# Performance work log

Hardware: AMD Instinct MI355X
Metric: run time of the kernel (lower is better)

The kernel has to match this reference:

```python
import jax, jax.numpy as jnp
import numpy as np

# ---- static geometry (matches init_kwargs) ----
B, S, D = 2, 4096, 2048
H, HD = 32, 64                      # num_heads, head_dim
HGRID, WGRID = 64, 64               # canvas h_dim, w_dim
TH, TW = 8, 16                      # tile size (th*tw = 128)
KH, KW = 16, 32                     # window (kernel) size
NTH, NTW = HGRID // TH, WGRID // TW
T = NTH * NTW                       # 32 tiles
TN = TH * TW                        # 128 tokens per tile
KTH, KTW = KH // TH, KW // TW
K = KTH * KTW                       # 4 kv tiles per query tile
SCALE = 1.0 / np.sqrt(HD)


def _kv_tile_ids():
    # For each query tile, the K kv tiles inside its (clamped) sliding window.
    qt = np.arange(T)
    qh, qw = qt // NTW, qt % NTW
    lbh, rbh = KTH // 2, KTH // 2 + (KTH % 2 - 1)
    lbw, rbw = KTW // 2, KTW // 2 + (KTW % 2 - 1)
    ch = np.clip(qh, lbh, NTH - 1 - rbh)
    cw = np.clip(qw, lbw, NTW - 1 - rbw)
    hh = ch[:, None] - lbh + np.arange(KTH)          # [T, KTH]
    ww = cw[:, None] - lbw + np.arange(KTW)          # [T, KTW]
    return (hh[:, :, None] * NTW + ww[:, None, :]).reshape(T, K)

KV_TILES = jnp.asarray(_kv_tile_ids())  # [T, K] int


def _to_tiles(x):
    # [B, S, H, HD] (row-major h,w) -> [B, H, T, TN, HD] (tile-major)
    x = x.reshape(B, NTH, TH, NTW, TW, H, HD)
    x = x.transpose(0, 5, 1, 3, 2, 4, 6)  # B,H,nth,ntw,th,tw,hd
    return x.reshape(B, H, T, TN, HD)


def _from_tiles(x):
    # [B, H, T, TN, HD] -> [B, S, H*HD]
    x = x.reshape(B, H, NTH, NTW, TH, TW, HD)
    x = x.transpose(0, 2, 4, 3, 5, 1, 6)  # B,nth,th,ntw,tw,H,hd
    return x.reshape(B, S, H * HD)


def setup_inputs() -> dict:
    key = jax.random.key(0)
    ks = jax.random.split(key, 5)
    sw = 1.0 / np.sqrt(D)
    return {
        "hidden_states": jax.random.normal(ks[0], (B, S, D), jnp.float32),
        "Wq": jax.random.normal(ks[1], (D, D), jnp.float32) * sw,
        "Wk": jax.random.normal(ks[2], (D, D), jnp.float32) * sw,
        "Wv": jax.random.normal(ks[3], (D, D), jnp.float32) * sw,
        "Wo": jax.random.normal(ks[4], (D, D), jnp.float32) * sw,
    }


def reference(hidden_states, Wq, Wk, Wv, Wo):
    # projections (weights stored [in, out]; equivalent to nn.Linear math)
    q = _to_tiles((hidden_states @ Wq).reshape(B, S, H, HD))  # [B,H,T,TN,HD]
    k = _to_tiles((hidden_states @ Wk).reshape(B, S, H, HD))
    v = _to_tiles((hidden_states @ Wv).reshape(B, S, H, HD))

    # gather the K allowed kv tiles for every query tile (block-sparse pattern)
    kg = k[:, :, KV_TILES].reshape(B, H, T, K * TN, HD)  # [B,H,T,K*TN,HD]
    vg = v[:, :, KV_TILES].reshape(B, H, T, K * TN, HD)

    # dense attention within each block (all gathered tokens are valid)
    scores = jnp.einsum("bhtqd,bhtkd->bhtqk", q, kg) * SCALE
    attn = jax.nn.softmax(scores, axis=-1)
    o = jnp.einsum("bhtqk,bhtkd->bhtqd", attn, vg)  # [B,H,T,TN,HD]

    return _from_tiles(o) @ Wo  # [B, S, D]
```

## Files before the change

### kernel.cpp

```cpp
#include <hip/hip_runtime.h>

typedef __bf16 bf16;
typedef __attribute__((ext_vector_type(8))) __bf16 bf16x8;
typedef __attribute__((ext_vector_type(4))) __bf16 bf16x4;
typedef __attribute__((ext_vector_type(4))) float f32x4;

#define MFMA16(a, b, c) __builtin_amdgcn_mfma_f32_16x16x32_bf16((a), (b), (c), 0, 0, 0)

__device__ __forceinline__ void gload16(const void* g, void* lds) {
  __builtin_amdgcn_global_load_lds(
      (__attribute__((address_space(1))) unsigned int*)(unsigned long long)g,
      (__attribute__((address_space(3))) unsigned int*)lds, 16, 0, 0);
}

__global__ void __launch_bounds__(256) cast_x_kernel(const float* __restrict__ X,
                                                     bf16* __restrict__ Xb) {
  int i = (blockIdx.x * 256 + threadIdx.x) * 4;
  f32x4 v = *(const f32x4*)(X + i);
  bf16x4 o;
  o[0] = (bf16)v[0]; o[1] = (bf16)v[1]; o[2] = (bf16)v[2]; o[3] = (bf16)v[3];
  *(bf16x4*)(Xb + i) = o;
}

__global__ void __launch_bounds__(256) transpose_w_kernel(const float* __restrict__ W,
                                                          bf16* __restrict__ WT) {
  __shared__ float tile[64][65];
  int n0 = (blockIdx.x & 31) * 64;
  int k0 = (blockIdx.x >> 5) * 64;
  int tid = threadIdx.x;
  int r = tid >> 4;
  int c4 = (tid & 15) * 4;
#pragma unroll
  for (int i = 0; i < 4; ++i) {
    f32x4 v = *(const f32x4*)(W + (size_t)(k0 + r + i * 16) * 2048 + n0 + c4);
    tile[r + i * 16][c4 + 0] = v[0];
    tile[r + i * 16][c4 + 1] = v[1];
    tile[r + i * 16][c4 + 2] = v[2];
    tile[r + i * 16][c4 + 3] = v[3];
  }
  __syncthreads();
#pragma unroll
  for (int i = 0; i < 4; ++i) {
    int n = r + i * 16;
    bf16x4 o;
    o[0] = (bf16)tile[c4 + 0][n];
    o[1] = (bf16)tile[c4 + 1][n];
    o[2] = (bf16)tile[c4 + 2][n];
    o[3] = (bf16)tile[c4 + 3][n];
    *(bf16x4*)(WT + (size_t)(n0 + n) * 2048 + k0 + c4) = o;
  }
}

__device__ __forceinline__ void gemm256_core(const bf16* __restrict__ Ag,
                                             const bf16* __restrict__ Bg,
                                             char* lds, f32x4 (&acc)[8][4]) {
  const int tid = threadIdx.x;
  const int lane = tid & 63, wid = tid >> 6;
  const int g = lane >> 4, r16 = lane & 15;
  const int wm = wid >> 2, wn = wid & 3;
  const int swz = ((g ^ ((r16 >> 1) & 3)) << 4);

  const int srow = wid * 32 + (lane >> 2);
  const int scol = ((lane & 3) ^ ((lane >> 3) & 3)) * 8;
  const bf16* gA = Ag + (size_t)srow * 2048 + scol;
  const bf16* gB = Bg + (size_t)srow * 2048 + scol;
  char* sA = lds + wid * 2048;
  char* sB = lds + 16384 + wid * 2048;

  const int arow0 = wm * 128 + r16;
  const int brow0 = wn * 64 + r16;

#define STAGE_A(bf_, tt_)                              \
  {                                                    \
    char* d_ = sA + (bf_) * 32768;                     \
    const bf16* s_ = gA + (size_t)(tt_) * 32;          \
    gload16(s_, d_);                                   \
    gload16(s_ + (size_t)16 * 2048, d_ + 1024);        \
  }
#define STAGE_B(bf_, tt_)                              \
  {                                                    \
    char* d_ = sB + (bf_) * 32768;                     \
    const bf16* s_ = gB + (size_t)(tt_) * 32;          \
    gload16(s_, d_);                                   \
    gload16(s_ + (size_t)16 * 2048, d_ + 1024);        \
  }

  STAGE_A(0, 0) STAGE_B(0, 0)
  STAGE_A(1, 1) STAGE_B(1, 1)
  STAGE_A(2, 2) STAGE_B(2, 2)
  asm volatile("s_waitcnt vmcnt(8)" ::: "memory");
  __builtin_amdgcn_s_barrier();
  __builtin_amdgcn_sched_barrier(0);

  for (int t = 0; t < 64; ++t) {
    const int c = t & 3;
    const char* Ab = lds + c * 32768;
    const char* Bb = Ab + 16384;
    const int sbuf = (c + 3) & 3;

    bf16x8 bfr[4], af[8];
#pragma unroll
    for (int j = 0; j < 4; ++j)
      bfr[j] = *(const bf16x8*)(Bb + (brow0 + j * 16) * 64 + swz);
#pragma unroll
    for (int i = 0; i < 8; ++i)
      af[i] = *(const bf16x8*)(Ab + (arow0 + i * 16) * 64 + swz);

    if (t <= 60) { STAGE_A(sbuf, t + 3) STAGE_B(sbuf, t + 3) }

#pragma unroll
    for (int i = 0; i < 8; ++i)
#pragma unroll
      for (int j = 0; j < 4; ++j)
        acc[i][j] = MFMA16(af[i], bfr[j], acc[i][j]);

    if (t <= 60) {
      asm volatile("s_waitcnt vmcnt(8)" ::: "memory");
    } else if (t == 61) {
      asm volatile("s_waitcnt vmcnt(4)" ::: "memory");
    } else if (t == 62) {
      asm volatile("s_waitcnt vmcnt(0)" ::: "memory");
    }
    __builtin_amdgcn_s_barrier();
    __builtin_amdgcn_sched_barrier(0);
  }
#undef STAGE_A
#undef STAGE_B
}

__global__ void __launch_bounds__(512, 2) gemm_qkv_kernel(
    const bf16* __restrict__ Xb, const bf16* __restrict__ W0, const bf16* __restrict__ W1,
    const bf16* __restrict__ W2, bf16* __restrict__ q_t, bf16* __restrict__ k_t,
    bf16* __restrict__ v_t) {
  __shared__ char lds[131072];
  int bid = blockIdx.x;
  int xcd = bid & 7, idx = bid >> 3;
  int by = xcd * 4 + idx / 24, bx = idx % 24;
  int which = bx >> 3;
  int m0 = by * 256, n0 = (bx & 7) * 256;
  const bf16* W = which == 0 ? W0 : (which == 1 ? W1 : W2);

  f32x4 acc[8][4] = {};
  gemm256_core(Xb + (size_t)m0 * 2048, W + (size_t)n0 * 2048, lds, acc);

  int lane = threadIdx.x & 63, wid = threadIdx.x >> 6;
  int g = lane >> 4, r16 = lane & 15;
  int wm = wid >> 2, wn = wid & 3;
#pragma unroll
  for (int i = 0; i < 8; ++i) {
#pragma unroll
    for (int r = 0; r < 4; ++r) {
      int m = m0 + wm * 128 + i * 16 + g * 4 + r;
      int b = m >> 12, s = m & 4095;
      int hg = s >> 6, wg = s & 63;
      int t = ((hg >> 3) << 2) + (wg >> 4);
      int tn = ((hg & 7) << 4) + (wg & 15);
#pragma unroll
      for (int j = 0; j < 4; ++j) {
        int n = n0 + wn * 64 + j * 16 + r16;
        int h = n >> 6, hd = n & 63;
        float val = acc[i][j][r];
        size_t base = ((size_t)(b * 32 + h) * 32 + t);
        if (which == 0)
          q_t[(base * 128 + tn) * 64 + hd] = (bf16)(val * 0.125f);
        else if (which == 1)
          k_t[(base * 128 + tn) * 64 + hd] = (bf16)val;
        else
          v_t[(base * 64 + hd) * 128 + tn] = (bf16)val;
      }
    }
  }
}

__global__ void __launch_bounds__(512, 2) gemm_out_kernel(const bf16* __restrict__ A,
                                                          const bf16* __restrict__ W,
                                                          float* __restrict__ C) {
  __shared__ char lds[131072];
  int bid = blockIdx.x;
  int xcd = bid & 7, idx = bid >> 3;
  int by = xcd * 4 + idx / 8, bx = idx & 7;
  int m0 = by * 256, n0 = bx * 256;

  f32x4 acc[8][4] = {};
  gemm256_core(A + (size_t)m0 * 2048, W + (size_t)n0 * 2048, lds, acc);

  int lane = threadIdx.x & 63, wid = threadIdx.x >> 6;
  int g = lane >> 4, r16 = lane & 15;
  int wm = wid >> 2, wn = wid & 3;
#pragma unroll
  for (int i = 0; i < 8; ++i)
#pragma unroll
    for (int j = 0; j < 4; ++j)
#pragma unroll
      for (int r = 0; r < 4; ++r) {
        int m = m0 + wm * 128 + i * 16 + g * 4 + r;
        int n = n0 + wn * 64 + j * 16 + r16;
        C[(size_t)m * 2048 + n] = acc[i][j][r];
      }
}

__global__ void __launch_bounds__(256) attn_kernel(const bf16* __restrict__ q_t,
                                                   const bf16* __restrict__ k_t,
                                                   const bf16* __restrict__ v_t,
                                                   bf16* __restrict__ o_bf) {
  __shared__ char Pl[128 * 256];
  int bid = blockIdx.x;
  int t = bid & 31, bh = bid >> 5;
  int h = bh & 31, b = bh >> 5;
  int tid = threadIdx.x, w = tid >> 6, lane = tid & 63;
  int g = lane >> 4, r16 = lane & 15;

  const size_t qoff = (size_t)bid * (128 * 64);
  bf16x8 qf[2][2];
#pragma unroll
  for (int mf = 0; mf < 2; ++mf)
#pragma unroll
    for (int kf = 0; kf < 2; ++kf)
      qf[mf][kf] = *(const bf16x8*)&q_t[qoff + (size_t)(w * 32 + mf * 16 + r16) * 64 + kf * 32 + g * 8];

  f32x4 oacc[2][4] = {};
  float mrun[2][4], lrun[2][4];
#pragma unroll
  for (int mf = 0; mf < 2; ++mf)
#pragma unroll
    for (int r = 0; r < 4; ++r) { mrun[mf][r] = -1e30f; lrun[mf][r] = 0.f; }

  int qh = t >> 2, qw = t & 3;
  int ch = qh < 1 ? 1 : (qh > 7 ? 7 : qh);
  int cw = qw < 1 ? 1 : (qw > 3 ? 3 : qw);

  for (int c = 0; c < 4; ++c) {
    int vt = (ch - 1 + (c >> 1)) * 4 + (cw - 1 + (c & 1));
    const bf16* Kt = k_t + ((size_t)bh * 32 + vt) * (128 * 64);
    const bf16* Vt = v_t + ((size_t)bh * 32 + vt) * (128 * 64);

    f32x4 s[2][8];
#pragma unroll
    for (int nf = 0; nf < 8; ++nf) {
      bf16x8 kf0 = *(const bf16x8*)&Kt[(nf * 16 + r16) * 64 + g * 8];
      bf16x8 kf1 = *(const bf16x8*)&Kt[(nf * 16 + r16) * 64 + 32 + g * 8];
#pragma unroll
      for (int mf = 0; mf < 2; ++mf) {
        f32x4 z = {};
        z = MFMA16(qf[mf][0], kf0, z);
        z = MFMA16(qf[mf][1], kf1, z);
        s[mf][nf] = z;
      }
    }

#pragma unroll
    for (int mf = 0; mf < 2; ++mf) {
#pragma unroll
      for (int r = 0; r < 4; ++r) {
        float mx = s[mf][0][r];
#pragma unroll
        for (int nf = 1; nf < 8; ++nf) mx = fmaxf(mx, s[mf][nf][r]);
        mx = fmaxf(mx, __shfl_xor(mx, 1));
        mx = fmaxf(mx, __shfl_xor(mx, 2));
        mx = fmaxf(mx, __shfl_xor(mx, 4));
        mx = fmaxf(mx, __shfl_xor(mx, 8));
        float mold = mrun[mf][r];
        float mnew = fmaxf(mold, mx);
        float sc = __expf(mold - mnew);
        mrun[mf][r] = mnew;
        float ps = 0.f;
#pragma unroll
        for (int nf = 0; nf < 8; ++nf) {
          float p = __expf(s[mf][nf][r] - mnew);
          s[mf][nf][r] = p;
          ps += p;
        }
        ps += __shfl_xor(ps, 1);
        ps += __shfl_xor(ps, 2);
        ps += __shfl_xor(ps, 4);
        ps += __shfl_xor(ps, 8);
        lrun[mf][r] = lrun[mf][r] * sc + ps;
#pragma unroll
        for (int hf = 0; hf < 4; ++hf) oacc[mf][hf][r] *= sc;
      }
    }

#pragma unroll
    for (int mf = 0; mf < 2; ++mf)
#pragma unroll
      for (int r = 0; r < 4; ++r) {
        int row = w * 32 + mf * 16 + g * 4 + r;
        int rb = row * 256;
        int swzp = (row & 7) << 4;
#pragma unroll
        for (int nf = 0; nf < 8; ++nf) {
          int addr = (rb + (nf * 16 + r16) * 2) ^ swzp;
          *(bf16*)(Pl + addr) = (bf16)s[mf][nf][r];
        }
      }
    __syncthreads();

#pragma unroll
    for (int ks = 0; ks < 4; ++ks) {
      bf16x8 pf[2];
#pragma unroll
      for (int mf = 0; mf < 2; ++mf) {
        int row = w * 32 + mf * 16 + r16;
        int addr = (row * 256 + ks * 64 + g * 16) ^ ((row & 7) << 4);
        pf[mf] = *(const bf16x8*)(Pl + addr);
      }
      bf16x8 vf[4];
#pragma unroll
      for (int hf = 0; hf < 4; ++hf)
        vf[hf] = *(const bf16x8*)&Vt[(hf * 16 + r16) * 128 + ks * 32 + g * 8];
#pragma unroll
      for (int mf = 0; mf < 2; ++mf)
#pragma unroll
        for (int hf = 0; hf < 4; ++hf)
          oacc[mf][hf] = MFMA16(pf[mf], vf[hf], oacc[mf][hf]);
    }
    __syncthreads();
  }

  int nth = t >> 2, ntw = t & 3;
#pragma unroll
  for (int mf = 0; mf < 2; ++mf)
#pragma unroll
    for (int r = 0; r < 4; ++r) {
      float inv = __builtin_amdgcn_rcpf(lrun[mf][r]);
      int tn = w * 32 + mf * 16 + g * 4 + r;
      int stok = (nth * 8 + (tn >> 4)) * 64 + ntw * 16 + (tn & 15);
#pragma unroll
      for (int hf = 0; hf < 4; ++hf) {
        int col = h * 64 + hf * 16 + r16;
        o_bf[((size_t)b * 4096 + stok) * 2048 + col] = (bf16)(oacc[mf][hf][r] * inv);
      }
    }
}

extern "C" void kernel_launch(void* const* d_in, const int* in_sizes, int n_in,
                              void* d_out, int out_size, void* d_ws, size_t ws_size,
                              hipStream_t stream) {
  const float* X = (const float*)d_in[0];
  const float* Wq = (const float*)d_in[1];
  const float* Wk = (const float*)d_in[2];
  const float* Wv = (const float*)d_in[3];
  const float* Wo = (const float*)d_in[4];
  float* out = (float*)d_out;
  char* ws = (char*)d_ws;
  if (ws_size < 159383552u) return;

  bf16* Xb  = (bf16*)(ws + 0);
  bf16* WT0 = (bf16*)(ws + 33554432u);
  bf16* WT1 = (bf16*)(ws + 41943040u);
  bf16* WT2 = (bf16*)(ws + 50331648u);
  bf16* q_t = (bf16*)(ws + 58720256u);
  bf16* k_t = (bf16*)(ws + 92274688u);
  bf16* v_t = (bf16*)(ws + 125829120u);
  bf16* o_bf = Xb;

  cast_x_kernel<<<16384, 256, 0, stream>>>(X, Xb);
  transpose_w_kernel<<<1024, 256, 0, stream>>>(Wq, WT0);
  transpose_w_kernel<<<1024, 256, 0, stream>>>(Wk, WT1);
  transpose_w_kernel<<<1024, 256, 0, stream>>>(Wv, WT2);
  gemm_qkv_kernel<<<768, 512, 0, stream>>>(Xb, WT0, WT1, WT2, q_t, k_t, v_t);
  attn_kernel<<<2048, 256, 0, stream>>>(q_t, k_t, v_t, o_bf);
  transpose_w_kernel<<<1024, 256, 0, stream>>>(Wo, WT0);
  gemm_out_kernel<<<256, 512, 0, stream>>>(o_bf, WT0, out);
}
```

Baseline: 512.4 us.

## Switch GEMM core to 32x32x16 MFMA with k64 double-buffered half-tile pipeline

```diff
diff --git a/kernel.cpp b/kernel.cpp
--- a/kernel.cpp
+++ b/kernel.cpp
@@ -4,8 +4,10 @@
 typedef __attribute__((ext_vector_type(8))) __bf16 bf16x8;
 typedef __attribute__((ext_vector_type(4))) __bf16 bf16x4;
 typedef __attribute__((ext_vector_type(4))) float f32x4;
+typedef __attribute__((ext_vector_type(16))) float f32x16;
 
 #define MFMA16(a, b, c) __builtin_amdgcn_mfma_f32_16x16x32_bf16((a), (b), (c), 0, 0, 0)
+#define MFMA32(a, b, c) __builtin_amdgcn_mfma_f32_32x32x16_bf16((a), (b), (c), 0, 0, 0)
 
 __device__ __forceinline__ void gload16(const void* g, void* lds) {
   __builtin_amdgcn_global_load_lds(
@@ -53,79 +55,93 @@
 
 __device__ __forceinline__ void gemm256_core(const bf16* __restrict__ Ag,
                                              const bf16* __restrict__ Bg,
-                                             char* lds, f32x4 (&acc)[8][4]) {
+                                             char* lds, f32x16 (&acc)[4][2]) {
   const int tid = threadIdx.x;
   const int lane = tid & 63, wid = tid >> 6;
-  const int g = lane >> 4, r16 = lane & 15;
+  const int l31 = lane & 31, l5 = lane >> 5;
   const int wm = wid >> 2, wn = wid & 3;
-  const int swz = ((g ^ ((r16 >> 1) & 3)) << 4);
-
-  const int srow = wid * 32 + (lane >> 2);
-  const int scol = ((lane & 3) ^ ((lane >> 3) & 3)) * 8;
-  const bf16* gA = Ag + (size_t)srow * 2048 + scol;
-  const bf16* gB = Bg + (size_t)srow * 2048 + scol;
-  char* sA = lds + wid * 2048;
-  char* sB = lds + 16384 + wid * 2048;
-
-  const int arow0 = wm * 128 + r16;
-  const int brow0 = wn * 64 + r16;
-
-#define STAGE_A(bf_, tt_)                              \
-  {                                                    \
-    char* d_ = sA + (bf_) * 32768;                     \
-    const bf16* s_ = gA + (size_t)(tt_) * 32;          \
-    gload16(s_, d_);                                   \
-    gload16(s_ + (size_t)16 * 2048, d_ + 1024);        \
-  }
-#define STAGE_B(bf_, tt_)                              \
-  {                                                    \
-    char* d_ = sB + (bf_) * 32768;                     \
-    const bf16* s_ = gB + (size_t)(tt_) * 32;          \
-    gload16(s_, d_);                                   \
-    gload16(s_ + (size_t)16 * 2048, d_ + 1024);        \
-  }
-
-  STAGE_A(0, 0) STAGE_B(0, 0)
-  STAGE_A(1, 1) STAGE_B(1, 1)
-  STAGE_A(2, 2) STAGE_B(2, 2)
-  asm volatile("s_waitcnt vmcnt(8)" ::: "memory");
+
+  const int srow = wid * 16 + (lane >> 2);
+  const int sg = ((lane & 3) ^ ((lane >> 3) & 3)) * 8;
+  const bf16* gA = Ag + (size_t)srow * 2048 + sg;
+  const bf16* gB = Bg + (size_t)srow * 2048 + sg;
+  char* sBase = lds + wid * 1024;
+
+  const int g01 = ((l5) ^ ((l31 >> 1) & 3)) * 16;
+  const int g23 = ((2 + l5) ^ ((l31 >> 1) & 3)) * 16;
+  const char* aB = lds + (wm * 128 + l31) * 64;
+  const char* bB = lds + 32768 + (wn * 64 + l31) * 64;
+
+#define STAGE(ab_, buf_, kh_, T_)                                        \
+  {                                                                      \
+    const bf16* s_ = ((ab_) ? gB : gA) + (size_t)(T_) * 64 + (kh_) * 32; \
+    char* d_ = sBase + (buf_) * 65536 + (ab_) * 32768 + (kh_) * 16384;   \
+    gload16(s_, d_);                                                     \
+    gload16(s_ + (size_t)128 * 2048, d_ + 8192);                         \
+  }
+
+#define LD6(buf_, kk_)                                                   \
+  {                                                                      \
+    const int kb_ = (buf_) * 65536 + ((kk_) >> 1) * 16384;               \
+    const int gb_ = ((kk_) & 1) ? g23 : g01;                             \
+    af0 = *(const bf16x8*)(aB + kb_ + 0 * 2048 + gb_);                   \
+    af1 = *(const bf16x8*)(aB + kb_ + 1 * 2048 + gb_);                   \
+    af2 = *(const bf16x8*)(aB + kb_ + 2 * 2048 + gb_);                   \
+    af3 = *(const bf16x8*)(aB + kb_ + 3 * 2048 + gb_);                   \
+    bq0 = *(const bf16x8*)(bB + kb_ + 0 * 2048 + gb_);                   \
+    bq1 = *(const bf16x8*)(bB + kb_ + 1 * 2048 + gb_);                   \
+  }
+
+#define MFMA_CLUSTER()                                                   \
+  __builtin_amdgcn_s_barrier();                                          \
+  asm volatile("s_waitcnt lgkmcnt(0)" ::: "memory");                     \
+  __builtin_amdgcn_sched_barrier(0);                                     \
+  __builtin_amdgcn_s_setprio(1);                                         \
+  acc[0][0] = MFMA32(af0, bq0, acc[0][0]);                               \
+  acc[0][1] = MFMA32(af0, bq1, acc[0][1]);                               \
+  acc[1][0] = MFMA32(af1, bq0, acc[1][0]);                               \
+  acc[1][1] = MFMA32(af1, bq1, acc[1][1]);                               \
+  acc[2][0] = MFMA32(af2, bq0, acc[2][0]);                               \
+  acc[2][1] = MFMA32(af2, bq1, acc[2][1]);                               \
+  acc[3][0] = MFMA32(af3, bq0, acc[3][0]);                               \
+  acc[3][1] = MFMA32(af3, bq1, acc[3][1]);                               \
+  __builtin_amdgcn_s_setprio(0);
+
+  bf16x8 af0, af1, af2, af3, bq0, bq1;
+
+  STAGE(0, 0, 0, 0) STAGE(1, 0, 0, 0)
+  STAGE(0, 0, 1, 0) STAGE(1, 0, 1, 0)
+  STAGE(0, 1, 0, 1) STAGE(1, 1, 0, 1)
+  asm volatile("s_waitcnt vmcnt(4)" ::: "memory");
   __builtin_amdgcn_s_barrier();
-  __builtin_amdgcn_sched_barrier(0);
-
-  for (int t = 0; t < 64; ++t) {
-    const int c = t & 3;
-    const char* Ab = lds + c * 32768;
-    const char* Bb = Ab + 16384;
-    const int sbuf = (c + 3) & 3;
-
-    bf16x8 bfr[4], af[8];
-#pragma unroll
-    for (int j = 0; j < 4; ++j)
-      bfr[j] = *(const bf16x8*)(Bb + (brow0 + j * 16) * 64 + swz);
-#pragma unroll
-    for (int i = 0; i < 8; ++i)
-      af[i] = *(const bf16x8*)(Ab + (arow0 + i * 16) * 64 + swz);
-
-    if (t <= 60) { STAGE_A(sbuf, t + 3) STAGE_B(sbuf, t + 3) }
-
-#pragma unroll
-    for (int i = 0; i < 8; ++i)
-#pragma unroll
-      for (int j = 0; j < 4; ++j)
-        acc[i][j] = MFMA16(af[i], bfr[j], acc[i][j]);
-
-    if (t <= 60) {
-      asm volatile("s_waitcnt vmcnt(8)" ::: "memory");
-    } else if (t == 61) {
-      asm volatile("s_waitcnt vmcnt(4)" ::: "memory");
-    } else if (t == 62) {
-      asm volatile("s_waitcnt vmcnt(0)" ::: "memory");
-    }
+
+  for (int t = 0; t < 32; t += 2) {
+    LD6(0, 0) if (t + 1 < 32) STAGE(0, 1, 1, t + 1)
+    MFMA_CLUSTER() __builtin_amdgcn_s_barrier();
+    LD6(0, 1) if (t + 1 < 32) STAGE(1, 1, 1, t + 1)
+    MFMA_CLUSTER() __builtin_amdgcn_s_barrier();
+    LD6(0, 2) if (t + 2 < 32) STAGE(0, 0, 0, t + 2)
+    MFMA_CLUSTER() __builtin_amdgcn_s_barrier();
+    LD6(0, 3) if (t + 2 < 32) STAGE(1, 0, 0, t + 2)
+    MFMA_CLUSTER()
+    if (t + 2 < 32) { asm volatile("s_waitcnt vmcnt(4)" ::: "memory"); }
+    else           { asm volatile("s_waitcnt vmcnt(0)" ::: "memory"); }
     __builtin_amdgcn_s_barrier();
-    __builtin_amdgcn_sched_barrier(0);
-  }
-#undef STAGE_A
-#undef STAGE_B
+    LD6(1, 0) if (t + 2 < 32) STAGE(0, 0, 1, t + 2)
+    MFMA_CLUSTER() __builtin_amdgcn_s_barrier();
+    LD6(1, 1) if (t + 2 < 32) STAGE(1, 0, 1, t + 2)
+    MFMA_CLUSTER() __builtin_amdgcn_s_barrier();
+    LD6(1, 2) if (t + 3 < 32) STAGE(0, 1, 0, t + 3)
+    MFMA_CLUSTER() __builtin_amdgcn_s_barrier();
+    LD6(1, 3) if (t + 3 < 32) STAGE(1, 1, 0, t + 3)
+    MFMA_CLUSTER()
+    if (t + 3 < 32) { asm volatile("s_waitcnt vmcnt(4)" ::: "memory"); }
+    else           { asm volatile("s_waitcnt vmcnt(0)" ::: "memory"); }
+    __builtin_amdgcn_s_barrier();
+  }
+#undef STAGE
+#undef LD6
+#undef MFMA_CLUSTER
 }
 
 __global__ void __launch_bounds__(512, 2) gemm_qkv_kernel(
@@ -140,27 +156,27 @@
   int m0 = by * 256, n0 = (bx & 7) * 256;
   const bf16* W = which == 0 ? W0 : (which == 1 ? W1 : W2);
 
-  f32x4 acc[8][4] = {};
+  f32x16 acc[4][2] = {};
   gemm256_core(Xb + (size_t)m0 * 2048, W + (size_t)n0 * 2048, lds, acc);
 
   int lane = threadIdx.x & 63, wid = threadIdx.x >> 6;
-  int g = lane >> 4, r16 = lane & 15;
+  int l31 = lane & 31, l5 = lane >> 5;
   int wm = wid >> 2, wn = wid & 3;
 #pragma unroll
-  for (int i = 0; i < 8; ++i) {
-#pragma unroll
-    for (int r = 0; r < 4; ++r) {
-      int m = m0 + wm * 128 + i * 16 + g * 4 + r;
+  for (int mi = 0; mi < 4; ++mi) {
+#pragma unroll
+    for (int reg = 0; reg < 16; ++reg) {
+      int m = m0 + wm * 128 + mi * 32 + (reg & 3) + ((reg >> 2) * 8) + l5 * 4;
       int b = m >> 12, s = m & 4095;
       int hg = s >> 6, wg = s & 63;
-      int t = ((hg >> 3) << 2) + (wg >> 4);
+      int tt = ((hg >> 3) << 2) + (wg >> 4);
       int tn = ((hg & 7) << 4) + (wg & 15);
 #pragma unroll
-      for (int j = 0; j < 4; ++j) {
-        int n = n0 + wn * 64 + j * 16 + r16;
+      for (int nj = 0; nj < 2; ++nj) {
+        int n = n0 + wn * 64 + nj * 32 + l31;
         int h = n >> 6, hd = n & 63;
-        float val = acc[i][j][r];
-        size_t base = ((size_t)(b * 32 + h) * 32 + t);
+        float val = acc[mi][nj][reg];
+        size_t base = ((size_t)(b * 32 + h) * 32 + tt);
         if (which == 0)
           q_t[(base * 128 + tn) * 64 + hd] = (bf16)(val * 0.125f);
         else if (which == 1)
@@ -181,21 +197,21 @@
   int by = xcd * 4 + idx / 8, bx = idx & 7;
   int m0 = by * 256, n0 = bx * 256;
 
-  f32x4 acc[8][4] = {};
+  f32x16 acc[4][2] = {};
   gemm256_core(A + (size_t)m0 * 2048, W + (size_t)n0 * 2048, lds, acc);
 
   int lane = threadIdx.x & 63, wid = threadIdx.x >> 6;
-  int g = lane >> 4, r16 = lane & 15;
+  int l31 = lane & 31, l5 = lane >> 5;
   int wm = wid >> 2, wn = wid & 3;
 #pragma unroll
-  for (int i = 0; i < 8; ++i)
-#pragma unroll
-    for (int j = 0; j < 4; ++j)
-#pragma unroll
-      for (int r = 0; r < 4; ++r) {
-        int m = m0 + wm * 128 + i * 16 + g * 4 + r;
-        int n = n0 + wn * 64 + j * 16 + r16;
-        C[(size_t)m * 2048 + n] = acc[i][j][r];
+  for (int mi = 0; mi < 4; ++mi)
+#pragma unroll
+    for (int nj = 0; nj < 2; ++nj)
+#pragma unroll
+      for (int reg = 0; reg < 16; ++reg) {
+        int m = m0 + wm * 128 + mi * 32 + (reg & 3) + ((reg >> 2) * 8) + l5 * 4;
+        int n = n0 + wn * 64 + nj * 32 + l31;
+        C[(size_t)m * 2048 + n] = acc[mi][nj][reg];
       }
 }
 
```

Result: slower. 542.0 us (+5.8%).
